# Optimization experiments

Measured on AMD Instinct MI355X. Metric: run time of the kernel, lower is better.

The kernel has to match this reference:

```python
import jax, jax.numpy as jnp
import numpy as np

EPS = 1e-5
K = 7        # deformable/spatial kernel size
GRID = 4     # local pool grid size


def conv(x, w, pad=0):
    # x: NCHW, w: OIHW
    return jax.lax.conv_general_dilated(
        x, w, (1, 1), [(pad, pad), (pad, pad)],
        dimension_numbers=('NCHW', 'OIHW', 'NCHW'))


def bn(x, g, b, m, v):
    # eval-mode batchnorm with running stats
    scale = (g * jax.lax.rsqrt(v + EPS))[None, :, None, None]
    return (x - m[None, :, None, None]) * scale + b[None, :, None, None]


def grid_sample(feat, grid):
    # bilinear, padding_mode='zeros', align_corners=False
    # feat: [b,c,h,w], grid: [b,h,w,2] with (x,y) in [-1,1]
    b, c, h, w = feat.shape
    gx = (grid[..., 0] + 1.0) * (w * 0.5) - 0.5
    gy = (grid[..., 1] + 1.0) * (h * 0.5) - 0.5
    x0 = jnp.floor(gx)
    y0 = jnp.floor(gy)
    wx = gx - x0
    wy = gy - y0
    feat_flat = feat.reshape(b, c, h * w)

    def gather(yi, xi):
        valid = (xi >= 0) & (xi < w) & (yi >= 0) & (yi < h)
        xi_c = jnp.clip(xi, 0, w - 1).astype(jnp.int32)
        yi_c = jnp.clip(yi, 0, h - 1).astype(jnp.int32)
        idx = (yi_c * w + xi_c).reshape(b, 1, h * w)
        vals = jnp.take_along_axis(feat_flat, idx, axis=2).reshape(b, c, h, w)
        return vals * valid[:, None].astype(feat.dtype)

    out = (gather(y0, x0) * ((1 - wx) * (1 - wy))[:, None]
           + gather(y0, x0 + 1) * (wx * (1 - wy))[:, None]
           + gather(y0 + 1, x0) * ((1 - wx) * wy)[:, None]
           + gather(y0 + 1, x0 + 1) * (wx * wy)[:, None])
    return out


def cmife_forward(x, align_w, align_g, align_b, align_m, align_v,
                  mlp_w1, mlp_w2, loc_w1, loc_w2, fusion_w,
                  off_w1, off_g, off_bt, off_m, off_v, off_w2, off_b2,
                  attn_w):
    # ---- align: 1x1 conv + BN + SiLU ----
    x = conv(x, align_w)
    x = bn(x, align_g, align_b, align_m, align_v)
    x = x * jax.nn.sigmoid(x)  # SiLU
    b_, c_, h_, w_ = x.shape

    # ---- LocalGlobalChannelAttention ----
    def mlp(z):
        return conv(jax.nn.relu(conv(z, mlp_w1)), mlp_w2)

    g_avg = mlp(jnp.mean(x, (2, 3), keepdims=True))
    g_max = mlp(jnp.max(x, (2, 3), keepdims=True))
    global_attn = g_avg + g_max
    # adaptive avg pool to GRIDxGRID (h,w divisible by GRID)
    loc = x.reshape(b_, c_, GRID, h_ // GRID, GRID, w_ // GRID).mean((3, 5))
    local_attn = conv(jax.nn.relu(conv(loc, loc_w1)), loc_w2)
    local_attn = local_attn.mean((2, 3), keepdims=True)
    alpha = jax.nn.sigmoid(fusion_w)
    ca = jax.nn.sigmoid(alpha * global_attn + (1 - alpha) * local_attn)
    x = ca * x

    # ---- DeformableSpatialAttention ----
    avg_out = jnp.mean(x, 1, keepdims=True)
    max_out = jnp.max(x, 1, keepdims=True)
    sf = jnp.concatenate([avg_out, max_out], axis=1)  # [b,2,h,w]
    o = jax.nn.relu(bn(conv(sf, off_w1, pad=1), off_g, off_bt, off_m, off_v))
    o = conv(o, off_w2, pad=1) + off_b2[None, :, None, None]  # [b,2*K*K,h,w]
    off = o.reshape(b_, 2, K * K, h_, w_).mean(2)             # [b,2,h,w]
    off = jnp.tanh(off) * 0.5
    off = jnp.transpose(off, (0, 2, 3, 1))                    # [b,h,w,2]
    gy, gx = jnp.meshgrid(jnp.linspace(-1.0, 1.0, h_),
                          jnp.linspace(-1.0, 1.0, w_), indexing='ij')
    base = jnp.stack([gx, gy], axis=-1)[None]                 # [1,h,w,2]
    dgrid = jnp.clip(base + off, -1.0, 1.0)
    sampled = grid_sample(sf, dgrid)                          # [b,2,h,w]
    sa = jax.nn.sigmoid(conv(sampled, attn_w, pad=K // 2))    # [b,1,h,w]
    return sa * x


def setup_inputs() -> dict:
    key = jax.random.key(0)
    ks = jax.random.split(key, 24)
    B, CIN, COUT, H, W, MID = 8, 256, 256, 160, 160, 16
    f = jnp.float32
    inp = {
        'x': jax.random.normal(ks[0], (B, CIN, H, W), f),
        'align_w': jax.random.normal(ks[1], (COUT, CIN, 1, 1), f) * 0.05,
        'align_g': jax.random.uniform(ks[2], (COUT,), f, 0.5, 1.5),
        'align_b': jax.random.normal(ks[3], (COUT,), f) * 0.1,
        'align_m': jax.random.normal(ks[4], (COUT,), f) * 0.1,
        'align_v': jax.random.uniform(ks[5], (COUT,), f, 0.5, 1.5),
        'mlp_w1': jax.random.normal(ks[6], (MID, COUT, 1, 1), f) * 0.1,
        'mlp_w2': jax.random.normal(ks[7], (COUT, MID, 1, 1), f) * 0.1,
        'loc_w1': jax.random.normal(ks[8], (MID, COUT, 1, 1), f) * 0.1,
        'loc_w2': jax.random.normal(ks[9], (COUT, MID, 1, 1), f) * 0.1,
        'fusion_w': jnp.float32(0.5),
        'off_w1': jax.random.normal(ks[10], (16, 2, 3, 3), f) * 0.1,
        'off_g': jax.random.uniform(ks[11], (16,), f, 0.5, 1.5),
        'off_bt': jax.random.normal(ks[12], (16,), f) * 0.1,
        'off_m': jax.random.normal(ks[13], (16,), f) * 0.1,
        'off_v': jax.random.uniform(ks[14], (16,), f, 0.5, 1.5),
        'off_w2': jax.random.normal(ks[15], (2 * K * K, 16, 3, 3), f) * 0.01,
        'off_b2': jax.random.normal(ks[16], (2 * K * K,), f) * 0.01,
        'attn_w': jax.random.normal(ks[17], (1, 2, K, K), f) * 0.1,
    }
    return inp


def reference(x, align_w, align_g, align_b, align_m, align_v,
              mlp_w1, mlp_w2, loc_w1, loc_w2, fusion_w,
              off_w1, off_g, off_bt, off_m, off_v, off_w2, off_b2,
              attn_w):
    return cmife_forward(x, align_w, align_g, align_b, align_m, align_v,
                         mlp_w1, mlp_w2, loc_w1, loc_w2, fusion_w,
                         off_w1, off_g, off_bt, off_m, off_v, off_w2, off_b2,
                         attn_w)
```

## Files before the change

### kernel.cpp

```cpp
#include <hip/hip_runtime.h>
#include <hip/hip_bf16.h>

#define HH 160
#define WW 160
#define HW 25600
#define NC 256
#define NB 8

typedef short short8 __attribute__((ext_vector_type(8)));
typedef float f32x4 __attribute__((ext_vector_type(4)));

__device__ __forceinline__ unsigned short f2bf(float f) {
    unsigned u = __float_as_uint(f);
    u += 0x7fffu + ((u >> 16) & 1u);
    return (unsigned short)(u >> 16);
}
__device__ __forceinline__ float bf2f(unsigned short h) {
    return __uint_as_float(((unsigned)h) << 16);
}

__global__ void k0_fold(const float* __restrict__ aw, const float* __restrict__ ag,
                        const float* __restrict__ ab, const float* __restrict__ am,
                        const float* __restrict__ av,
                        unsigned short* __restrict__ wpkh, unsigned short* __restrict__ wpkl,
                        float* __restrict__ biasp) {
    int co = blockIdx.x, t = threadIdx.x;
    float sc = ag[co] * rsqrtf(av[co] + 1e-5f);
    float w = aw[co * 256 + t] * sc;
    unsigned short h = f2bf(w);
    int kk = t >> 5, kq = t & 31;
    wpkh[kk * 10240 + co * 40 + kq] = h;
    wpkl[kk * 10240 + co * 40 + kq] = f2bf(w - bf2f(h));
    if (t == 0) biasp[co] = ab[co] - am[co] * sc;
}

__global__ void k0b_fold2(const float* __restrict__ ow2, const float* __restrict__ ob2,
                          float* __restrict__ weff, float* __restrict__ beff) {
    int t = threadIdx.x;
    if (t < 288) {
        int g = t / 144, r = t - g * 144;
        float s = 0.f;
        for (int q = 0; q < 49; q++) s += ow2[(size_t)(g * 49 + q) * 144 + r];
        weff[t] = s * (1.f / 49.f);
    }
    if (t < 2) {
        float s = 0.f;
        for (int q = 0; q < 49; q++) s += ob2[t * 49 + q];
        beff[t] = s * (1.f / 49.f);
    }
}

__global__ __launch_bounds__(512, 4) void k1_gemm(
    const float* __restrict__ X, const unsigned short* __restrict__ Wph,
    const unsigned short* __restrict__ Wpl,
    const float* __restrict__ biasp, float* __restrict__ xal) {
    __shared__ __align__(16) unsigned short Ah[10240];
    __shared__ __align__(16) unsigned short Al[10240];
    __shared__ __align__(16) unsigned short Bh[5120];
    __shared__ __align__(16) unsigned short Bl[5120];

    int t = threadIdx.x;
    int n0 = blockIdx.x * 128;
    int b  = blockIdx.y;
    const float* Xb = X + (size_t)b * NC * HW;

    int lane = t & 63, wv = t >> 6;
    int lcol = lane & 15, lq = lane >> 4;

    f32x4 acc[2][8];
#pragma unroll
    for (int i = 0; i < 2; i++)
#pragma unroll
        for (int j = 0; j < 8; j++) { f32x4 z = {0.f, 0.f, 0.f, 0.f}; acc[i][j] = z; }

    int bn  = t & 127;
    int kq2 = t >> 7;

    float pf[8];

    {
        const float* src = Xb + (size_t)(kq2 * 8) * HW + n0 + bn;
#pragma unroll
        for (int j = 0; j < 8; j++) pf[j] = src[(size_t)j * HW];
    }
    {
        const char* gah = (const char*)Wph;
        const char* gal = (const char*)Wpl;
#pragma unroll
        for (int i = 0; i < 3; i++) {
            if (i < 2 || wv < 4) {
                int off = i * 8192 + wv * 1024;
                __builtin_amdgcn_global_load_lds(
                    (const __attribute__((address_space(1))) unsigned int*)(gah + off + lane * 16),
                    (__attribute__((address_space(3))) unsigned int*)((char*)Ah + off),
                    16, 0, 0);
                __builtin_amdgcn_global_load_lds(
                    (const __attribute__((address_space(1))) unsigned int*)(gal + off + lane * 16),
                    (__attribute__((address_space(3))) unsigned int*)((char*)Al + off),
                    16, 0, 0);
            }
        }
    }

    for (int kk = 0; kk < 8; kk++) {
        {
            unsigned hi[4], lo[4];
#pragma unroll
            for (int j = 0; j < 4; j++) {
                unsigned short a = f2bf(pf[2 * j]);
                unsigned short c = f2bf(pf[2 * j + 1]);
                hi[j] = (unsigned)a | ((unsigned)c << 16);
                unsigned short la = f2bf(pf[2 * j] - bf2f(a));
                unsigned short lc = f2bf(pf[2 * j + 1] - bf2f(c));
                lo[j] = (unsigned)la | ((unsigned)lc << 16);
            }
            *(uint4*)(&Bh[bn * 40 + kq2 * 8]) = make_uint4(hi[0], hi[1], hi[2], hi[3]);
            *(uint4*)(&Bl[bn * 40 + kq2 * 8]) = make_uint4(lo[0], lo[1], lo[2], lo[3]);
        }
        __syncthreads();

        short8 afh[2], afl[2];
#pragma unroll
        for (int mt = 0; mt < 2; mt++) {
            afh[mt] = *(const short8*)(&Ah[(wv * 32 + mt * 16 + lcol) * 40 + lq * 8]);
            afl[mt] = *(const short8*)(&Al[(wv * 32 + mt * 16 + lcol) * 40 + lq * 8]);
        }
        if (kk < 7) {
            const float* src = Xb + (size_t)((kk + 1) * 32 + kq2 * 8) * HW + n0 + bn;
#pragma unroll
            for (int j = 0; j < 8; j++) pf[j] = src[(size_t)j * HW];
        }
#pragma unroll
        for (int nt = 0; nt < 8; nt++) {
            short8 bh = *(const short8*)(&Bh[(nt * 16 + lcol) * 40 + lq * 8]);
            short8 bl = *(const short8*)(&Bl[(nt * 16 + lcol) * 40 + lq * 8]);
#pragma unroll
            for (int mt = 0; mt < 2; mt++) {
                acc[mt][nt] = __builtin_amdgcn_mfma_f32_16x16x32_bf16(
                    afh[mt], bh, acc[mt][nt], 0, 0, 0);
                acc[mt][nt] = __builtin_amdgcn_mfma_f32_16x16x32_bf16(
                    afh[mt], bl, acc[mt][nt], 0, 0, 0);
                acc[mt][nt] = __builtin_amdgcn_mfma_f32_16x16x32_bf16(
                    afl[mt], bh, acc[mt][nt], 0, 0, 0);
            }
        }
        asm volatile("s_barrier" ::: "memory");
        if (kk < 7) {
            const char* gah = (const char*)(Wph + (kk + 1) * 10240);
            const char* gal = (const char*)(Wpl + (kk + 1) * 10240);
#pragma unroll
            for (int i = 0; i < 3; i++) {
                if (i < 2 || wv < 4) {
                    int off = i * 8192 + wv * 1024;
                    __builtin_amdgcn_global_load_lds(
                        (const __attribute__((address_space(1))) unsigned int*)(gah + off + lane * 16),
                        (__attribute__((address_space(3))) unsigned int*)((char*)Ah + off),
                        16, 0, 0);
                    __builtin_amdgcn_global_load_lds(
                        (const __attribute__((address_space(1))) unsigned int*)(gal + off + lane * 16),
                        (__attribute__((address_space(3))) unsigned int*)((char*)Al + off),
                        16, 0, 0);
                }
            }
        }
    }
#pragma unroll
    for (int mt = 0; mt < 2; mt++) {
#pragma unroll
        for (int r = 0; r < 4; r++) {
            int co = wv * 32 + mt * 16 + lq * 4 + r;
            float bias = biasp[co];
            size_t rowbase = ((size_t)b * NC + co) * HW + n0;
#pragma unroll
            for (int nt = 0; nt < 8; nt++) {
                int n = nt * 16 + lcol;
                float y = acc[mt][nt][r] + bias;
                float z = y / (1.f + __expf(-y));
                xal[rowbase + n] = z;
            }
        }
    }
}

__global__ void ka_stats(const float* __restrict__ xal,
                         float* __restrict__ cellsum, float* __restrict__ cellmax) {
    __shared__ float rs[320], rm[320];
    int blk = blockIdx.x;
    int bc = blk >> 2, band = blk & 3;
    const float* base = xal + (size_t)bc * HW + band * 6400;
    int t = threadIdx.x;
    int col = (t % 40) / 10;
    float s = 0.f, m = -3.4e38f;
#pragma unroll
    for (int i = 0; i < 5; i++) {
        f32x4 v = *(const f32x4*)(base + (size_t)(i * 320 + t) * 4);
        s += (v[0] + v[1]) + (v[2] + v[3]);
        m = fmaxf(fmaxf(fmaxf(m, v[0]), fmaxf(v[1], v[2])), v[3]);
    }
    int slot = (t / 40) * 10 + (t % 10);
    rs[col * 80 + slot] = s;
    rm[col * 80 + slot] = m;
    __syncthreads();
    if (t < 64) {
#pragma unroll
        for (int c2 = 0; c2 < 4; c2++) {
            float sv = rs[c2 * 80 + t] + ((t < 16) ? rs[c2 * 80 + 64 + t] : 0.f);
            float mv = fmaxf(rm[c2 * 80 + t],
                             (t < 16) ? rm[c2 * 80 + 64 + t] : -3.4e38f);
#pragma unroll
            for (int off = 32; off >= 1; off >>= 1) {
                sv += __shfl_down(sv, off, 64);
                mv = fmaxf(mv, __shfl_down(mv, off, 64));
            }
            if (t == 0) {
                cellsum[bc * 16 + band * 4 + c2] = sv;
                cellmax[bc * 16 + band * 4 + c2] = mv;
            }
        }
    }
}

__global__ void kb_attn(const float* __restrict__ cellsum, const float* __restrict__ cellmax,
                        const float* __restrict__ mw1, const float* __restrict__ mw2,
                        const float* __restrict__ lw1, const float* __restrict__ lw2,
                        const float* __restrict__ fw, float* __restrict__ ca) {
    __shared__ float avgS[256], maxS[256], locS[256 * 16], hid[32], hlS[256];
    int b = blockIdx.x, t = threadIdx.x;
    float s = 0.f, m = -3.4e38f;
#pragma unroll
    for (int cell = 0; cell < 16; cell++) {
        float cs = cellsum[(b * 256 + t) * 16 + cell];
        float cm = cellmax[(b * 256 + t) * 16 + cell];
        s += cs;
        m = fmaxf(m, cm);
        locS[t * 16 + cell] = cs * (1.f / 1600.f);
    }
    avgS[t] = s * (1.f / 25600.f);
    maxS[t] = m;
    __syncthreads();
    if (t < 32) {
        int j = t & 15;
        const float* w1 = mw1 + j * 256;
        const float* src = (t < 16) ? avgS : maxS;
        float h = 0.f;
        for (int c = 0; c < 256; c++) h += w1[c] * src[c];
        hid[t] = fmaxf(h, 0.f);
    }
    {
        int cell = t >> 4, j = t & 15;
        const float* w1 = lw1 + j * 256;
        float h = 0.f;
        for (int c = 0; c < 256; c++) h += w1[c] * locS[c * 16 + cell];
        hlS[t] = fmaxf(h, 0.f);
    }
    __syncthreads();
    float ga = 0.f, gm = 0.f;
#pragma unroll
    for (int j = 0; j < 16; j++) {
        float w2 = mw2[t * 16 + j];
        ga += w2 * hid[j];
        gm += w2 * hid[16 + j];
    }
    float la = 0.f;
#pragma unroll
    for (int cell = 0; cell < 16; cell++)
#pragma unroll
        for (int j = 0; j < 16; j++)
            la += lw2[t * 16 + j] * hlS[cell * 16 + j];
    float alpha = 1.f / (1.f + expf(-fw[0]));
    float pre = alpha * (ga + gm) + (1.f - alpha) * (la * (1.f / 16.f));
    ca[b * 256 + t] = 1.f / (1.f + expf(-pre));
}

__global__ void k3_sf(const float* __restrict__ xal,
                      const float* __restrict__ ca, float* __restrict__ sf) {
    __shared__ float cas[256];
    int b = blockIdx.y, t = threadIdx.x;
    cas[t] = ca[b * 256 + t];
    __syncthreads();
    int p = blockIdx.x * 256 + t;
    const float* base = xal + (size_t)b * NC * HW + p;
    float s0 = 0.f, m0 = -3.4e38f;
    for (int c = 0; c < 256; c++) {
        float a0 = cas[c] * base[(size_t)c * HW];
        s0 += a0;
        m0 = fmaxf(m0, a0);
    }
    sf[(size_t)b * 2 * HW + p]      = s0 * (1.f / 256.f);
    sf[(size_t)b * 2 * HW + HW + p] = m0;
}

__global__ void k4_conv1(const float* __restrict__ sf, const float* __restrict__ ow1,
                         const float* __restrict__ og, const float* __restrict__ obt,
                         const float* __restrict__ om, const float* __restrict__ ov,
                         float* __restrict__ o1) {
    __shared__ float wS[288], scS[16], shS[16];
    int b = blockIdx.y, t = threadIdx.x;
    for (int i = t; i < 288; i += 256) wS[i] = ow1[i];
    if (t < 16) {
        float sc = og[t] * rsqrtf(ov[t] + 1e-5f);
        scS[t] = sc;
        shS[t] = obt[t] - om[t] * sc;
    }
    __syncthreads();
    int p = blockIdx.x * 256 + t;
    int h = p / 160, w = p - h * 160;
    const float* a0 = sf + (size_t)b * 2 * HW;
    const float* a1 = a0 + HW;
    float in0[9], in1[9];
#pragma unroll
    for (int kh = 0; kh < 3; kh++)
#pragma unroll
        for (int kw = 0; kw < 3; kw++) {
            int hh = h + kh - 1, ww = w + kw - 1;
            bool ok = (hh >= 0) & (hh < 160) & (ww >= 0) & (ww < 160);
            int q = hh * 160 + ww;
            in0[kh * 3 + kw] = ok ? a0[q] : 0.f;
            in1[kh * 3 + kw] = ok ? a1[q] : 0.f;
        }
    float* outb = o1 + (size_t)b * 16 * HW + p;
#pragma unroll
    for (int j = 0; j < 16; j++) {
        float acc = 0.f;
#pragma unroll
        for (int k = 0; k < 9; k++)
            acc += wS[j * 18 + k] * in0[k] + wS[j * 18 + 9 + k] * in1[k];
        outb[(size_t)j * HW] = fmaxf(acc * scS[j] + shS[j], 0.f);
    }
}

__global__ void k5_sample(const float* __restrict__ o1, const float* __restrict__ weff,
                          const float* __restrict__ beff, const float* __restrict__ sf,
                          float* __restrict__ sampled) {
    __shared__ float tileS[16 * 18 * 18];
    __shared__ float wS[288];
    __shared__ float bS[2];
    int b = blockIdx.y, t = threadIdx.x;
    int ty0 = (blockIdx.x / 10) * 16, tx0 = (blockIdx.x % 10) * 16;
    const float* ob = o1 + (size_t)b * 16 * HW;
    for (int i = t; i < 288; i += 256) wS[i] = weff[i];
    if (t < 2) bS[t] = beff[t];
    for (int i = t; i < 16 * 18 * 18; i += 256) {
        int ci = i / 324, rem = i - ci * 324;
        int r = rem / 18, c = rem - r * 18;
        int gr = ty0 + r - 1, gc = tx0 + c - 1;
        bool ok = (gr >= 0) & (gr < 160) & (gc >= 0) & (gc < 160);
        tileS[i] = ok ? ob[(size_t)ci * HW + gr * 160 + gc] : 0.f;
    }
    __syncthreads();
    int ty = t >> 4, tx = t & 15;
    int h = ty0 + ty, w = tx0 + tx;
    int p = h * 160 + w;
    float s0 = bS[0], s1 = bS[1];
#pragma unroll
    for (int ci = 0; ci < 16; ci++) {
        const float* tb = &tileS[ci * 324 + ty * 18 + tx];
        const float* w0 = &wS[ci * 9];
        const float* w1 = &wS[144 + ci * 9];
#pragma unroll
        for (int kh = 0; kh < 3; kh++)
#pragma unroll
            for (int kw = 0; kw < 3; kw++) {
                float v = tb[kh * 18 + kw];
                s0 += w0[kh * 3 + kw] * v;
                s1 += w1[kh * 3 + kw] * v;
            }
    }
    float ox = tanhf(s0) * 0.5f;
    float oy = tanhf(s1) * 0.5f;
    float bx = w * (2.f / 159.f) - 1.f, by = h * (2.f / 159.f) - 1.f;
    float gxn = fminf(fmaxf(bx + ox, -1.f), 1.f);
    float gyn = fminf(fmaxf(by + oy, -1.f), 1.f);
    float gx = (gxn + 1.f) * 80.f - 0.5f;
    float gy = (gyn + 1.f) * 80.f - 0.5f;
    float x0f = floorf(gx), y0f = floorf(gy);
    float wx = gx - x0f, wy = gy - y0f;
    int ix0 = (int)x0f, iy0 = (int)y0f;
    const float* f0 = sf + (size_t)b * 2 * HW;
    const float* f1 = f0 + HW;
    float r0 = 0.f, r1 = 0.f;
#pragma unroll
    for (int dy = 0; dy < 2; dy++)
#pragma unroll
        for (int dx = 0; dx < 2; dx++) {
            int xi = ix0 + dx, yi = iy0 + dy;
            float wgt = (dx ? wx : 1.f - wx) * (dy ? wy : 1.f - wy);
            if ((xi >= 0) & (xi < 160) & (yi >= 0) & (yi < 160)) {
                int q = yi * 160 + xi;
                r0 += wgt * f0[q];
                r1 += wgt * f1[q];
            }
        }
    float* sb = sampled + (size_t)b * 2 * HW + p;
    sb[0] = r0;
    sb[HW] = r1;
}

__global__ void k5b_sa(const float* __restrict__ sampled, const float* __restrict__ attn_w,
                       float* __restrict__ sa) {
    __shared__ float wS[98];
    int b = blockIdx.y, t = threadIdx.x;
    if (t < 98) wS[t] = attn_w[t];
    __syncthreads();
    int p = blockIdx.x * 256 + t;
    int h = p / 160, w = p - h * 160;
    const float* s0 = sampled + (size_t)b * 2 * HW;
    const float* s1 = s0 + HW;
    float acc = 0.f;
#pragma unroll
    for (int kh = 0; kh < 7; kh++) {
        int hh = h + kh - 3;
        if (hh < 0 || hh >= 160) continue;
#pragma unroll
        for (int kw = 0; kw < 7; kw++) {
            int ww = w + kw - 3;
            if (ww < 0 || ww >= 160) continue;
            int q = hh * 160 + ww;
            acc += wS[kh * 7 + kw] * s0[q] + wS[49 + kh * 7 + kw] * s1[q];
        }
    }
    sa[(size_t)b * HW + p] = 1.f / (1.f + expf(-acc));
}

__global__ void k6_out(float* __restrict__ out, const float* __restrict__ ca,
                       const float* __restrict__ sa) {
    unsigned e4 = blockIdx.x * 256 + threadIdx.x;
    unsigned e = e4 * 4;
    unsigned b = e / (256u * HW);
    unsigned rem = e - b * (256u * HW);
    unsigned c = rem / HW;
    unsigned p = rem - c * HW;
    f32x4 v = *(f32x4*)(out + e);
    f32x4 s = *(const f32x4*)(sa + (size_t)b * HW + p);
    float cav = ca[b * 256 + c];
#pragma unroll
    for (int i = 0; i < 4; i++) v[i] = cav * s[i] * v[i];
    *(f32x4*)(out + e) = v;
}

extern "C" void kernel_launch(void* const* d_in, const int* in_sizes, int n_in,
                              void* d_out, int out_size, void* d_ws, size_t ws_size,
                              hipStream_t stream) {
    const float* x       = (const float*)d_in[0];
    const float* align_w = (const float*)d_in[1];
    const float* align_g = (const float*)d_in[2];
    const float* align_b = (const float*)d_in[3];
    const float* align_m = (const float*)d_in[4];
    const float* align_v = (const float*)d_in[5];
    const float* mlp_w1  = (const float*)d_in[6];
    const float* mlp_w2  = (const float*)d_in[7];
    const float* loc_w1  = (const float*)d_in[8];
    const float* loc_w2  = (const float*)d_in[9];
    const float* fusion  = (const float*)d_in[10];
    const float* off_w1  = (const float*)d_in[11];
    const float* off_g   = (const float*)d_in[12];
    const float* off_bt  = (const float*)d_in[13];
    const float* off_m   = (const float*)d_in[14];
    const float* off_v   = (const float*)d_in[15];
    const float* off_w2  = (const float*)d_in[16];
    const float* off_b2  = (const float*)d_in[17];
    const float* attn_w  = (const float*)d_in[18];
    float* out = (float*)d_out;

    char* wsb = (char*)d_ws;
    size_t off = 0;
    auto alloc = [&](size_t bytes) -> void* {
        off = (off + 255) & ~(size_t)255;
        void* p = wsb + off;
        off += bytes;
        return p;
    };
    float* xal = out;
    unsigned short* wph = (unsigned short*)alloc(81920 * 2);
    unsigned short* wpl = (unsigned short*)alloc(81920 * 2);
    float* biasp   = (float*)alloc(256 * 4);
    float* cellsum = (float*)alloc(32768 * 4);
    float* cellmax = (float*)alloc(32768 * 4);
    float* ca      = (float*)alloc(2048 * 4);
    float* sf      = (float*)alloc((size_t)NB * 2 * HW * 4);
    float* o1      = (float*)alloc((size_t)NB * 16 * HW * 4);
    float* sampled = (float*)alloc((size_t)NB * 2 * HW * 4);
    float* sa      = (float*)alloc((size_t)NB * HW * 4);
    float* weff    = (float*)alloc(288 * 4);
    float* beff    = (float*)alloc(2 * 4);
    (void)ws_size; (void)in_sizes; (void)n_in; (void)out_size;

    k0_fold<<<dim3(256), 256, 0, stream>>>(align_w, align_g, align_b, align_m, align_v,
                                           wph, wpl, biasp);
    k0b_fold2<<<dim3(1), 320, 0, stream>>>(off_w2, off_b2, weff, beff);
    k1_gemm<<<dim3(200, 8), 512, 0, stream>>>(x, wph, wpl, biasp, xal);
    ka_stats<<<dim3(8192), 320, 0, stream>>>(xal, cellsum, cellmax);
    kb_attn<<<dim3(8), 256, 0, stream>>>(cellsum, cellmax, mlp_w1, mlp_w2,
                                         loc_w1, loc_w2, fusion, ca);
    k3_sf<<<dim3(100, 8), 256, 0, stream>>>(xal, ca, sf);
    k4_conv1<<<dim3(100, 8), 256, 0, stream>>>(sf, off_w1, off_g, off_bt, off_m, off_v, o1);
    k5_sample<<<dim3(100, 8), 256, 0, stream>>>(o1, weff, beff, sf, sampled);
    k5b_sa<<<dim3(100, 8), 256, 0, stream>>>(sampled, attn_w, sa);
    k6_out<<<dim3(51200), 256, 0, stream>>>(out, ca, sa);
}
```

Before: 708.6 us.

## Fuse offset conv1 into sampling kernel and relax GEMM launch bounds

Merges the 3x3 offset conv+BN+ReLU kernel into the sampling kernel. Each block loads a 20x20 halo of the pooled features and computes the 16-channel 18x18 intermediate tile in shared memory, so the 16-channel intermediate buffer is never written to or read from global memory. This recomputes halo pixels across neighbouring blocks. Separately, the GEMM's min-blocks-per-CU launch bound drops from 4 to 2, giving the compiler more registers at the cost of possible occupancy.

```diff
diff --git a/kernel.cpp b/kernel.cpp
--- a/kernel.cpp
+++ b/kernel.cpp
@@ -50,7 +50,7 @@
     }
 }
 
-__global__ __launch_bounds__(512, 4) void k1_gemm(
+__global__ __launch_bounds__(512, 2) void k1_gemm(
     const float* __restrict__ X, const unsigned short* __restrict__ Wph,
     const unsigned short* __restrict__ Wpl,
     const float* __restrict__ biasp, float* __restrict__ xal) {
@@ -290,62 +290,50 @@
     sf[(size_t)b * 2 * HW + HW + p] = m0;
 }
 
-__global__ void k4_conv1(const float* __restrict__ sf, const float* __restrict__ ow1,
-                         const float* __restrict__ og, const float* __restrict__ obt,
-                         const float* __restrict__ om, const float* __restrict__ ov,
-                         float* __restrict__ o1) {
-    __shared__ float wS[288], scS[16], shS[16];
+__global__ void k45_sample(const float* __restrict__ sf, const float* __restrict__ ow1,
+                           const float* __restrict__ og, const float* __restrict__ obt,
+                           const float* __restrict__ om, const float* __restrict__ ov,
+                           const float* __restrict__ weff, const float* __restrict__ beff,
+                           float* __restrict__ sampled) {
+    __shared__ float sfS[800];
+    __shared__ float tileS[16 * 18 * 18];
+    __shared__ float w1S[288], scS[16], shS[16];
+    __shared__ float wS[288];
+    __shared__ float bS[2];
     int b = blockIdx.y, t = threadIdx.x;
-    for (int i = t; i < 288; i += 256) wS[i] = ow1[i];
+    int ty0 = (blockIdx.x / 10) * 16, tx0 = (blockIdx.x % 10) * 16;
+    const float* f0 = sf + (size_t)b * 2 * HW;
+    const float* f1 = f0 + HW;
+    for (int i = t; i < 288; i += 256) { w1S[i] = ow1[i]; wS[i] = weff[i]; }
     if (t < 16) {
         float sc = og[t] * rsqrtf(ov[t] + 1e-5f);
         scS[t] = sc;
         shS[t] = obt[t] - om[t] * sc;
     }
-    __syncthreads();
-    int p = blockIdx.x * 256 + t;
-    int h = p / 160, w = p - h * 160;
-    const float* a0 = sf + (size_t)b * 2 * HW;
-    const float* a1 = a0 + HW;
-    float in0[9], in1[9];
-#pragma unroll
-    for (int kh = 0; kh < 3; kh++)
-#pragma unroll
-        for (int kw = 0; kw < 3; kw++) {
-            int hh = h + kh - 1, ww = w + kw - 1;
-            bool ok = (hh >= 0) & (hh < 160) & (ww >= 0) & (ww < 160);
-            int q = hh * 160 + ww;
-            in0[kh * 3 + kw] = ok ? a0[q] : 0.f;
-            in1[kh * 3 + kw] = ok ? a1[q] : 0.f;
-        }
-    float* outb = o1 + (size_t)b * 16 * HW + p;
-#pragma unroll
-    for (int j = 0; j < 16; j++) {
-        float acc = 0.f;
-#pragma unroll
-        for (int k = 0; k < 9; k++)
-            acc += wS[j * 18 + k] * in0[k] + wS[j * 18 + 9 + k] * in1[k];
-        outb[(size_t)j * HW] = fmaxf(acc * scS[j] + shS[j], 0.f);
-    }
-}
-
-__global__ void k5_sample(const float* __restrict__ o1, const float* __restrict__ weff,
-                          const float* __restrict__ beff, const float* __restrict__ sf,
-                          float* __restrict__ sampled) {
-    __shared__ float tileS[16 * 18 * 18];
-    __shared__ float wS[288];
-    __shared__ float bS[2];
-    int b = blockIdx.y, t = threadIdx.x;
-    int ty0 = (blockIdx.x / 10) * 16, tx0 = (blockIdx.x % 10) * 16;
-    const float* ob = o1 + (size_t)b * 16 * HW;
-    for (int i = t; i < 288; i += 256) wS[i] = weff[i];
     if (t < 2) bS[t] = beff[t];
-    for (int i = t; i < 16 * 18 * 18; i += 256) {
+    for (int i = t; i < 800; i += 256) {
+        int ch = i / 400, rem = i - ch * 400;
+        int r = rem / 20, c = rem - r * 20;
+        int gr = ty0 + r - 2, gc = tx0 + c - 2;
+        bool ok = (gr >= 0) & (gr < 160) & (gc >= 0) & (gc < 160);
+        sfS[i] = ok ? f0[(size_t)ch * HW + gr * 160 + gc] : 0.f;
+    }
+    __syncthreads();
+    for (int i = t; i < 16 * 324; i += 256) {
         int ci = i / 324, rem = i - ci * 324;
         int r = rem / 18, c = rem - r * 18;
         int gr = ty0 + r - 1, gc = tx0 + c - 1;
+        float acc = 0.f;
+#pragma unroll
+        for (int kh = 0; kh < 3; kh++)
+#pragma unroll
+            for (int kw = 0; kw < 3; kw++) {
+                int k = kh * 3 + kw;
+                acc += w1S[ci * 18 + k]     * sfS[(r + kh) * 20 + (c + kw)]
+                     + w1S[ci * 18 + 9 + k] * sfS[400 + (r + kh) * 20 + (c + kw)];
+            }
         bool ok = (gr >= 0) & (gr < 160) & (gc >= 0) & (gc < 160);
-        tileS[i] = ok ? ob[(size_t)ci * HW + gr * 160 + gc] : 0.f;
+        tileS[i] = ok ? fmaxf(acc * scS[ci] + shS[ci], 0.f) : 0.f;
     }
     __syncthreads();
     int ty = t >> 4, tx = t & 15;
@@ -376,8 +364,6 @@
     float x0f = floorf(gx), y0f = floorf(gy);
     float wx = gx - x0f, wy = gy - y0f;
     int ix0 = (int)x0f, iy0 = (int)y0f;
-    const float* f0 = sf + (size_t)b * 2 * HW;
-    const float* f1 = f0 + HW;
     float r0 = 0.f, r1 = 0.f;
 #pragma unroll
     for (int dy = 0; dy < 2; dy++)
@@ -478,7 +464,6 @@
     float* cellmax = (float*)alloc(32768 * 4);
     float* ca      = (float*)alloc(2048 * 4);
     float* sf      = (float*)alloc((size_t)NB * 2 * HW * 4);
-    float* o1      = (float*)alloc((size_t)NB * 16 * HW * 4);
     float* sampled = (float*)alloc((size_t)NB * 2 * HW * 4);
     float* sa      = (float*)alloc((size_t)NB * HW * 4);
     float* weff    = (float*)alloc(288 * 4);
@@ -493,8 +478,8 @@
     kb_attn<<<dim3(8), 256, 0, stream>>>(cellsum, cellmax, mlp_w1, mlp_w2,
                                          loc_w1, loc_w2, fusion, ca);
     k3_sf<<<dim3(100, 8), 256, 0, stream>>>(xal, ca, sf);
-    k4_conv1<<<dim3(100, 8), 256, 0, stream>>>(sf, off_w1, off_g, off_bt, off_m, off_v, o1);
-    k5_sample<<<dim3(100, 8), 256, 0, stream>>>(o1, weff, beff, sf, sampled);
+    k45_sample<<<dim3(100, 8), 256, 0, stream>>>(sf, off_w1, off_g, off_bt, off_m, off_v,
+                                                 weff, beff, sampled);
     k5b_sa<<<dim3(100, 8), 256, 0, stream>>>(sampled, attn_w, sa);
     k6_out<<<dim3(51200), 256, 0, stream>>>(out, ca, sa);
 }
```

Result: no change. 706.0 us (-0.4%).
